# Performance work log

Measured on AMD Instinct MI355X. Metric: run time of the kernel, lower is better.

Reference implementation:

```python
import jax, jax.numpy as jnp
import numpy as np

WIN = 7
NP_ = WIN * WIN
COV_NORM = NP_ / (NP_ - 1)

def _box(x, w):
    # valid 7x7 box filter, NCHW, single channel
    return jax.lax.conv_general_dilated(
        x, w, window_strides=(1, 1), padding='VALID',
        dimension_numbers=('NCHW', 'OIHW', 'NCHW'))

def setup_inputs() -> dict:
    key = jax.random.key(0)
    k1, k2, k3, k4 = jax.random.split(key, 4)
    N, H, W = 64, 384, 384
    X = jax.random.uniform(k1, (N, 1, H, W), dtype=jnp.float32)
    Y = jax.random.uniform(k2, (N, 1, H, W), dtype=jnp.float32)
    norm = jax.random.uniform(k3, (N,), dtype=jnp.float32)
    mx = jax.random.uniform(k4, (N,), dtype=jnp.float32) + 0.5
    w = jnp.ones((1, 1, WIN, WIN), dtype=jnp.float32) / NP_
    return {"X": X, "Y": Y, "norm": norm, "max": mx, "w": w}

def reference(X, Y, norm, max, w):
    q = 100000.0
    X = X * q
    Y = Y * q
    mx = max * q
    data_range = mx[:, None, None, None]
    C1 = (0.01 * data_range) ** 2
    C2 = (0.03 * data_range) ** 2
    ux = _box(X, w)
    uy = _box(Y, w)
    uxx = _box(X * X, w)
    uyy = _box(Y * Y, w)
    uxy = _box(X * Y, w)
    vx = COV_NORM * (uxx - ux * ux)
    vy = COV_NORM * (uyy - uy * uy)
    vxy = COV_NORM * (uxy - ux * uy)
    A1 = 2 * ux * uy + C1
    A2 = 2 * vxy + C2
    B1 = ux ** 2 + uy ** 2 + C1
    B2 = vx + vy + C2
    S = (A1 * A2) / (B1 * B2)
    return -jnp.mean(S)
```

## Files before the change

kernel.cpp:

```cpp
#include <hip/hip_runtime.h>


constexpr int IND   = 384;
constexpr int OUTD  = 378;
constexpr int RB    = 9;
constexpr int BANDS = OUTD / RB;
constexpr int CPL   = 6;

using f32x2 = __attribute__((ext_vector_type(2))) float;

__global__ __launch_bounds__(64, 3)
void ssim_band(const float* __restrict__ X, const float* __restrict__ Y,
               const float* __restrict__ MX, float* __restrict__ blocksum)
{
    const int band = blockIdx.x;
    const int n    = blockIdx.y;
    const int lane = threadIdx.x;
    const int c0   = lane * CPL;
    const int r0   = band * RB;

    const float* __restrict__ Xp = X + (size_t)n * (IND * IND) + c0;
    const float* __restrict__ Yp = Y + (size_t)n * (IND * IND) + c0;

#define LOADROW(DX, DY, R) {                                                  \
    const float* _px = Xp + (size_t)(R) * IND;                                \
    const float* _py = Yp + (size_t)(R) * IND;                                \
    f32x2 _a = *(const f32x2*)_px;                                            \
    f32x2 _b = *(const f32x2*)(_px + 2);                                      \
    f32x2 _c = *(const f32x2*)(_px + 4);                                      \
    f32x2 _d = *(const f32x2*)_py;                                            \
    f32x2 _e = *(const f32x2*)(_py + 2);                                      \
    f32x2 _f = *(const f32x2*)(_py + 4);                                      \
    DX[0]=_a.x; DX[1]=_a.y; DX[2]=_b.x; DX[3]=_b.y; DX[4]=_c.x; DX[5]=_c.y;   \
    DY[0]=_d.x; DY[1]=_d.y; DY[2]=_e.x; DY[3]=_e.y; DY[4]=_f.x; DY[5]=_f.y; }

    float hx[7][CPL], hy[7][CPL];
#pragma unroll
    for (int k = 0; k < 6; ++k) LOADROW(hx[k], hy[k], r0 + k)

    float pax[CPL], pay[CPL], pbx[CPL], pby[CPL];
    LOADROW(pax, pay, r0 + 6)
    LOADROW(pbx, pby, r0 + 7)

    float sx[CPL]  = {}, sy[CPL]  = {};
    float sxx[CPL] = {}, syy[CPL] = {}, sxy[CPL] = {};
#pragma unroll
    for (int k = 0; k < 6; ++k)
#pragma unroll
        for (int c = 0; c < CPL; ++c) {
            float x = hx[k][c], y = hy[k][c];
            sx[c] += x;  sy[c] += y;
            sxx[c] = fmaf(x, x, sxx[c]);
            syy[c] = fmaf(y, y, syy[c]);
            sxy[c] = fmaf(x, y, sxy[c]);
        }

    const float m   = MX[n];
    const float c1  = (0.01f * m) * (0.01f * m);
    const float c2  = (0.03f * m) * (0.03f * m);
    const float k1  = 2401.0f * c1;
    const float k2  = 2401.0f * c2;
    const float cn  = 49.0f / 48.0f;
    const float cn2 = 2.0f * cn;

#define HSUM(S, O) {                                                          \
    float _n0 = __shfl_down(S[0], 1), _n1 = __shfl_down(S[1], 1);             \
    float _n2 = __shfl_down(S[2], 1), _n3 = __shfl_down(S[3], 1);             \
    float _n4 = __shfl_down(S[4], 1), _n5 = __shfl_down(S[5], 1);             \
    float _t  = ((S[0]+S[1]) + (S[2]+S[3])) + (S[4]+S[5]);                    \
    O[0] = _t   + _n0;                                                        \
    O[1] = O[0] - S[0] + _n1;                                                 \
    O[2] = O[1] - S[1] + _n2;                                                 \
    O[3] = O[2] - S[2] + _n3;                                                 \
    O[4] = O[3] - S[3] + _n4;                                                 \
    O[5] = O[4] - S[4] + _n5; }

    float partial = 0.f;

#pragma unroll
    for (int i = 0; i < RB; ++i) {
        const int ws = (i + 6) % 7;
        const int os = i % 7;

#pragma unroll
        for (int c = 0; c < CPL; ++c) {
            float nx = pax[c], ny = pay[c];
            sx[c] += nx;  sy[c] += ny;
            sxx[c] = fmaf(nx, nx, sxx[c]);
            syy[c] = fmaf(ny, ny, syy[c]);
            sxy[c] = fmaf(nx, ny, sxy[c]);
            hx[ws][c] = nx;  hy[ws][c] = ny;
        }

        float t1[CPL], t2[CPL], t5[CPL], u[CPL], t34[CPL];
        HSUM(sx,  t1) HSUM(sy,  t2) HSUM(sxy, t5)
#pragma unroll
        for (int c = 0; c < CPL; ++c) u[c] = sxx[c] + syy[c];
        HSUM(u, t34)

        if (lane < 63) {
#pragma unroll
            for (int c = 0; c < CPL; ++c) {
                float pxy = t1[c] * t2[c];
                float ss  = fmaf(t1[c], t1[c], t2[c] * t2[c]);
                float A1  = fmaf(2.f, pxy, k1);
                float B1  = ss + k1;
                float A2  = fmaf(cn2, fmaf(49.f, t5[c], -pxy), k2);
                float B2  = fmaf(cn, fmaf(49.f, t34[c], -ss), k2);
                partial += __fdividef(A1 * A2, B1 * B2);
            }
        }

#pragma unroll
        for (int c = 0; c < CPL; ++c) {
            float ox = hx[os][c], oy = hy[os][c];
            sx[c] -= ox;  sy[c] -= oy;
            sxx[c] = fmaf(-ox, ox, sxx[c]);
            syy[c] = fmaf(-oy, oy, syy[c]);
            sxy[c] = fmaf(-ox, oy, sxy[c]);
            pax[c] = pbx[c];  pay[c] = pby[c];
        }
        {
            int nr = r0 + 8 + i;  if (nr > IND - 1) nr = IND - 1;
            LOADROW(pbx, pby, nr)
        }
    }
#undef HSUM
#undef LOADROW

#pragma unroll
    for (int off = 32; off; off >>= 1) partial += __shfl_down(partial, off);
    if (lane == 0) blocksum[(size_t)n * BANDS + band] = partial;
}

__global__ __launch_bounds__(256)
void ssim_reduce(const float* __restrict__ blocksum, float* __restrict__ out,
                 int nblocks, float inv_npix)
{
    const int tid = threadIdx.x;
    float s = 0.f;
    for (int i = tid; i < nblocks; i += 256) s += blocksum[i];
#pragma unroll
    for (int off = 32; off; off >>= 1) s += __shfl_down(s, off);
    __shared__ float ws[4];
    if ((tid & 63) == 0) ws[tid >> 6] = s;
    __syncthreads();
    if (tid == 0) out[0] = -(ws[0] + ws[1] + ws[2] + ws[3]) * inv_npix;
}

extern "C" void kernel_launch(void* const* d_in, const int* in_sizes, int n_in,
                              void* d_out, int out_size, void* d_ws, size_t ws_size,
                              hipStream_t stream)
{
    const float* X  = (const float*)d_in[0];
    const float* Y  = (const float*)d_in[1];
    const float* MX = (const float*)d_in[3];

    const int N       = in_sizes[3];
    const int nblocks = N * BANDS;

    float* bs = (float*)d_ws;

    dim3 grid(BANDS, N);
    ssim_band<<<grid, 64, 0, stream>>>(X, Y, MX, bs);

    const float inv_npix = 1.0f / ((float)N * OUTD * OUTD);
    ssim_reduce<<<1, 256, 0, stream>>>(bs, (float*)d_out, nblocks, inv_npix);
}
```

Before: 35.35 us.

## Enlarge row bands, rework horizontal window sums via prefix/suffix shuffles

```diff
diff --git a/kernel.cpp b/kernel.cpp
--- a/kernel.cpp
+++ b/kernel.cpp
@@ -3,13 +3,13 @@
 
 constexpr int IND   = 384;
 constexpr int OUTD  = 378;
-constexpr int RB    = 9;
+constexpr int RB    = 14;
 constexpr int BANDS = OUTD / RB;
 constexpr int CPL   = 6;
 
 using f32x2 = __attribute__((ext_vector_type(2))) float;
 
-__global__ __launch_bounds__(64, 3)
+__global__ __launch_bounds__(64, 2)
 void ssim_band(const float* __restrict__ X, const float* __restrict__ Y,
                const float* __restrict__ MX, float* __restrict__ blocksum)
 {
@@ -21,6 +21,10 @@
 
     const float* __restrict__ Xp = X + (size_t)n * (IND * IND) + c0;
     const float* __restrict__ Yp = Y + (size_t)n * (IND * IND) + c0;
+
+    float hx[7][CPL], hy[7][CPL];
+    float sx[CPL]  = {}, sy[CPL]  = {};
+    float sxx[CPL] = {}, syy[CPL] = {}, sxy[CPL] = {};
 
 #define LOADROW(DX, DY, R) {                                                  \
     const float* _px = Xp + (size_t)(R) * IND;                                \
@@ -34,7 +38,6 @@
     DX[0]=_a.x; DX[1]=_a.y; DX[2]=_b.x; DX[3]=_b.y; DX[4]=_c.x; DX[5]=_c.y;   \
     DY[0]=_d.x; DY[1]=_d.y; DY[2]=_e.x; DY[3]=_e.y; DY[4]=_f.x; DY[5]=_f.y; }
 
-    float hx[7][CPL], hy[7][CPL];
 #pragma unroll
     for (int k = 0; k < 6; ++k) LOADROW(hx[k], hy[k], r0 + k)
 
@@ -42,8 +45,6 @@
     LOADROW(pax, pay, r0 + 6)
     LOADROW(pbx, pby, r0 + 7)
 
-    float sx[CPL]  = {}, sy[CPL]  = {};
-    float sxx[CPL] = {}, syy[CPL] = {}, sxy[CPL] = {};
 #pragma unroll
     for (int k = 0; k < 6; ++k)
 #pragma unroll
@@ -63,69 +64,90 @@
     const float cn  = 49.0f / 48.0f;
     const float cn2 = 2.0f * cn;
 
-#define HSUM(S, O) {                                                          \
-    float _n0 = __shfl_down(S[0], 1), _n1 = __shfl_down(S[1], 1);             \
-    float _n2 = __shfl_down(S[2], 1), _n3 = __shfl_down(S[3], 1);             \
-    float _n4 = __shfl_down(S[4], 1), _n5 = __shfl_down(S[5], 1);             \
-    float _t  = ((S[0]+S[1]) + (S[2]+S[3])) + (S[4]+S[5]);                    \
-    O[0] = _t   + _n0;                                                        \
-    O[1] = O[0] - S[0] + _n1;                                                 \
-    O[2] = O[1] - S[1] + _n2;                                                 \
-    O[3] = O[2] - S[2] + _n3;                                                 \
-    O[4] = O[3] - S[3] + _n4;                                                 \
-    O[5] = O[4] - S[4] + _n5; }
+#define PHASE_A(S, NP, CS) {                                                  \
+    float _p1 = S[0];                                                         \
+    float _p2 = _p1 + S[1];                                                   \
+    float _p3 = _p2 + S[2];                                                   \
+    float _p4 = _p3 + S[3];                                                   \
+    float _p5 = _p4 + S[4];                                                   \
+    float _p6 = _p5 + S[5];                                                   \
+    NP[0] = __shfl_down(_p1, 1);                                              \
+    NP[1] = __shfl_down(_p2, 1);                                              \
+    NP[2] = __shfl_down(_p3, 1);                                              \
+    NP[3] = __shfl_down(_p4, 1);                                              \
+    NP[4] = __shfl_down(_p5, 1);                                              \
+    NP[5] = __shfl_down(_p6, 1);                                              \
+    CS[5] = S[5];                                                             \
+    CS[4] = S[4] + S[5];                                                      \
+    CS[3] = S[3] + CS[4];                                                     \
+    CS[2] = S[2] + CS[3];                                                     \
+    CS[1] = S[1] + CS[2];                                                     \
+    CS[0] = _p6; }
 
     float partial = 0.f;
 
+#pragma unroll 1
+    for (int kk = 0; kk < RB / 7; ++kk) {
 #pragma unroll
-    for (int i = 0; i < RB; ++i) {
-        const int ws = (i + 6) % 7;
-        const int os = i % 7;
+        for (int i = 0; i < 7; ++i) {
+            const int os = i;
+            const int ws = (i + 6) % 7;
 
 #pragma unroll
-        for (int c = 0; c < CPL; ++c) {
-            float nx = pax[c], ny = pay[c];
-            sx[c] += nx;  sy[c] += ny;
-            sxx[c] = fmaf(nx, nx, sxx[c]);
-            syy[c] = fmaf(ny, ny, syy[c]);
-            sxy[c] = fmaf(nx, ny, sxy[c]);
-            hx[ws][c] = nx;  hy[ws][c] = ny;
-        }
+            for (int c = 0; c < CPL; ++c) {
+                float nx = pax[c], ny = pay[c];
+                sx[c] += nx;  sy[c] += ny;
+                sxx[c] = fmaf(nx, nx, sxx[c]);
+                syy[c] = fmaf(ny, ny, syy[c]);
+                sxy[c] = fmaf(nx, ny, sxy[c]);
+            }
+            float u[CPL];
+#pragma unroll
+            for (int c = 0; c < CPL; ++c) u[c] = sxx[c] + syy[c];
 
-        float t1[CPL], t2[CPL], t5[CPL], u[CPL], t34[CPL];
-        HSUM(sx,  t1) HSUM(sy,  t2) HSUM(sxy, t5)
-#pragma unroll
-        for (int c = 0; c < CPL; ++c) u[c] = sxx[c] + syy[c];
-        HSUM(u, t34)
+            float np1[CPL], np2[CPL], np5[CPL], np34[CPL];
+            float cs1[CPL], cs2[CPL], cs5[CPL], cs34[CPL];
+            PHASE_A(sx,  np1,  cs1)
+            PHASE_A(sy,  np2,  cs2)
+            PHASE_A(sxy, np5,  cs5)
+            PHASE_A(u,   np34, cs34)
 
-        if (lane < 63) {
 #pragma unroll
             for (int c = 0; c < CPL; ++c) {
-                float pxy = t1[c] * t2[c];
-                float ss  = fmaf(t1[c], t1[c], t2[c] * t2[c]);
-                float A1  = fmaf(2.f, pxy, k1);
-                float B1  = ss + k1;
-                float A2  = fmaf(cn2, fmaf(49.f, t5[c], -pxy), k2);
-                float B2  = fmaf(cn, fmaf(49.f, t34[c], -ss), k2);
-                partial += __fdividef(A1 * A2, B1 * B2);
+                float ox = hx[os][c], oy = hy[os][c];
+                float nx = pax[c],    ny = pay[c];
+                sx[c] -= ox;  sy[c] -= oy;
+                sxx[c] = fmaf(-ox, ox, sxx[c]);
+                syy[c] = fmaf(-oy, oy, syy[c]);
+                sxy[c] = fmaf(-ox, oy, sxy[c]);
+                hx[ws][c] = nx;  hy[ws][c] = ny;
+                pax[c] = pbx[c]; pay[c] = pby[c];
+            }
+            {
+                int nr = r0 + 7 * kk + i + 8;
+                if (nr > IND - 1) nr = IND - 1;
+                LOADROW(pbx, pby, nr)
+            }
+
+            if (lane < 63) {
+#pragma unroll
+                for (int c = 0; c < CPL; ++c) {
+                    float t1  = cs1[c]  + np1[c];
+                    float t2  = cs2[c]  + np2[c];
+                    float t5  = cs5[c]  + np5[c];
+                    float t34 = cs34[c] + np34[c];
+                    float pxy = t1 * t2;
+                    float ss  = fmaf(t1, t1, t2 * t2);
+                    float A1  = fmaf(2.f, pxy, k1);
+                    float B1  = ss + k1;
+                    float A2  = fmaf(cn2, fmaf(49.f, t5, -pxy), k2);
+                    float B2  = fmaf(cn, fmaf(49.f, t34, -ss), k2);
+                    partial += __fdividef(A1 * A2, B1 * B2);
+                }
             }
         }
-
-#pragma unroll
-        for (int c = 0; c < CPL; ++c) {
-            float ox = hx[os][c], oy = hy[os][c];
-            sx[c] -= ox;  sy[c] -= oy;
-            sxx[c] = fmaf(-ox, ox, sxx[c]);
-            syy[c] = fmaf(-oy, oy, syy[c]);
-            sxy[c] = fmaf(-ox, oy, sxy[c]);
-            pax[c] = pbx[c];  pay[c] = pby[c];
-        }
-        {
-            int nr = r0 + 8 + i;  if (nr > IND - 1) nr = IND - 1;
-            LOADROW(pbx, pby, nr)
-        }
     }
-#undef HSUM
+#undef PHASE_A
 #undef LOADROW
 
 #pragma unroll
```

Result: faster. 29.13 us (-17.6%).
